# Kernel tuning notes

Hardware: AMD Instinct MI355X
Metric: run time of the kernel (lower is better)

## Reference

```python
import jax, jax.numpy as jnp
import numpy as np

N_NODES = 100000
N_EDGES = 1600000


def setup_inputs() -> dict:
    key = jax.random.key(0)
    ks = jax.random.split(key, 6)
    x = jax.random.normal(ks[0], (N_NODES, 128), dtype=jnp.float32)
    edge_index = jax.random.randint(ks[1], (2, N_EDGES), 0, N_NODES, dtype=jnp.int64)
    # glorot-ish scaled weights
    W0 = jax.random.normal(ks[2], (128, 64), dtype=jnp.float32) * (1.0 / np.sqrt(128))
    W1 = jax.random.normal(ks[3], (64, 64), dtype=jnp.float32) * (1.0 / np.sqrt(64))
    W2 = jax.random.normal(ks[4], (64, 40), dtype=jnp.float32) * (1.0 / np.sqrt(64))
    b0 = jnp.zeros((64,), jnp.float32)
    b1 = jnp.zeros((64,), jnp.float32)
    b2 = jnp.zeros((40,), jnp.float32)
    return {"x": x, "edge_index": edge_index, "W0": W0, "b0": b0,
            "W1": W1, "b1": b1, "W2": W2, "b2": b2}


def _gcn_norm(edge_index, n, dtype):
    # PyG gcn_norm: add self-loops, deg over targets, norm = d^-1/2[src]*d^-1/2[dst]
    loop = jnp.arange(n, dtype=edge_index.dtype)
    src = jnp.concatenate([edge_index[0], loop])
    dst = jnp.concatenate([edge_index[1], loop])
    deg = jax.ops.segment_sum(jnp.ones_like(dst, dtype=dtype), dst, num_segments=n)
    dinv = jnp.where(deg > 0, jax.lax.rsqrt(deg), 0.0)
    return src, dst, dinv[src] * dinv[dst]


def reference(x, edge_index, W0, b0, W1, b1, W2, b2):
    n = x.shape[0]
    src, dst, norm = _gcn_norm(edge_index, n, x.dtype)

    def conv(h, W, b):
        h = h @ W                                   # [N, out]
        msg = h[src] * norm[:, None]                # gather + per-edge scale
        return jax.ops.segment_sum(msg, dst, num_segments=n) + b

    # dropout skipped (eval mode); relu between layers per forward()
    h = jax.nn.relu(conv(x, W0, b0))
    h = jax.nn.relu(conv(h, W1, b1))
    return conv(h, W2, b2)
```

## Files before the change

### kernel.cpp

```cpp
#include <hip/hip_runtime.h>
#include <hip/hip_fp16.h>


#define ALIGN256(x) (((size_t)(x) + 255) & ~(size_t)255)

typedef _Float16 f16;
typedef f16 f16x8 __attribute__((ext_vector_type(8)));
typedef float f32x4 __attribute__((ext_vector_type(4)));


__global__ __launch_bounds__(256) void k_coarse(const int* __restrict__ ei,
                                                int* __restrict__ ccnt,
                                                int* __restrict__ done,
                                                int* __restrict__ cbase,
                                                int* __restrict__ cpos,
                                                int* __restrict__ row_start,
                                                int E, int N, int NBUK, int nblk) {
    __shared__ int h[512];
    __shared__ int lastblk;
    int t = threadIdx.x;
    for (int i = t; i < NBUK; i += 256) h[i] = 0;
    __syncthreads();
    int e0 = blockIdx.x * 8192;
    int e1 = min(e0 + 8192, E);
    for (int e = e0 + t; e < e1; e += 256) atomicAdd(&h[ei[E + e] >> 8], 1);
    __syncthreads();
    for (int i = t; i < NBUK; i += 256) {
        int c = h[i];
        if (c) atomicAdd(&ccnt[i], c);
    }
    __threadfence();
    if (t == 0) lastblk = (atomicAdd(done, 1) == nblk - 1) ? 1 : 0;
    __syncthreads();
    if (!lastblk) return;

    __shared__ int sd[256];
    int i0 = 2 * t, i1 = 2 * t + 1;
    int v0 = (i0 < NBUK) ? ccnt[i0] : 0;
    int v1 = (i1 < NBUK) ? ccnt[i1] : 0;
    int s = v0 + v1;
    sd[t] = s;
    __syncthreads();
    for (int off = 1; off < 256; off <<= 1) {
        int u = (t >= off) ? sd[t - off] : 0;
        __syncthreads();
        sd[t] += u;
        __syncthreads();
    }
    int base = sd[t] - s;
    if (i0 < NBUK) { cbase[i0] = base;      cpos[i0] = base; }
    if (i1 < NBUK) { cbase[i1] = base + v0; cpos[i1] = base + v0; }
    if (t == 0) { cbase[NBUK] = E; row_start[N] = E; }
}


__global__ __launch_bounds__(256) void k_passA(const int* __restrict__ ei,
                                               int* __restrict__ cpos,
                                               unsigned int* __restrict__ stage,
                                               int E, int NBUK) {
    __shared__ int h[512];
    __shared__ int base[512];
    int t = threadIdx.x;
    for (int i = t; i < NBUK; i += 256) h[i] = 0;
    __syncthreads();
    int e0 = blockIdx.x * 8192;
    int e1 = min(e0 + 8192, E);
    for (int e = e0 + t; e < e1; e += 256) atomicAdd(&h[ei[E + e] >> 8], 1);
    __syncthreads();
    for (int b = t; b < NBUK; b += 256) {
        int c = h[b];
        base[b] = c ? atomicAdd(&cpos[b], c) : 0;
        h[b] = 0;
    }
    __syncthreads();
    for (int e = e0 + t; e < e1; e += 256) {
        unsigned int s = (unsigned int)ei[e];
        int d = ei[E + e];
        int b = d >> 8;
        int off = base[b] + atomicAdd(&h[b], 1);
        stage[off] = ((unsigned int)(d & 255) << 24) | s;
    }
}


__global__ __launch_bounds__(256) void k_B1(const unsigned int* __restrict__ stage,
                                            const int* __restrict__ cbase,
                                            int* __restrict__ row_start,
                                            float* __restrict__ dinv, int N) {
    __shared__ int cnt[256];
    __shared__ int sd[256];
    int b = blockIdx.x;
    int n0 = b << 8;
    int t = threadIdx.x;
    cnt[t] = 0;
    __syncthreads();
    int s0 = cbase[b], s1 = cbase[b + 1];
    for (int j = s0 + t; j < s1; j += 256) atomicAdd(&cnt[stage[j] >> 24], 1);
    __syncthreads();
    int c = cnt[t];
    sd[t] = c;
    __syncthreads();
    for (int off = 1; off < 256; off <<= 1) {
        int u = (t >= off) ? sd[t - off] : 0;
        __syncthreads();
        sd[t] += u;
        __syncthreads();
    }
    int excl = sd[t] - c;
    int node = n0 + t;
    if (node < N) {
        row_start[node] = s0 + excl;
        dinv[node] = 1.0f / sqrtf((float)(c + 1));
    }
}


__global__ __launch_bounds__(256) void k_B2(const unsigned int* __restrict__ stage,
                                            const int* __restrict__ cbase,
                                            const int* __restrict__ row_start,
                                            const float* __restrict__ dinv,
                                            int2* __restrict__ ep, int N) {
    __shared__ int lpos[256];
    __shared__ float ld[256];
    int b = blockIdx.x;
    int n0 = b << 8;
    int t = threadIdx.x;
    int node = n0 + t;
    if (node < N) {
        lpos[t] = row_start[node];
        ld[t] = dinv[node];
    }
    __syncthreads();
    int s0 = cbase[b], s1 = cbase[b + 1];
    for (int j = s0 + t; j < s1; j += 256) {
        unsigned int v = stage[j];
        int li = v >> 24;
        int src = v & 0xFFFFFF;
        int slot = atomicAdd(&lpos[li], 1);
        ep[slot] = make_int2(src, __float_as_int(dinv[src] * ld[li]));
    }
}


template <int K, int OUT, int NF, typename XT>
__global__ __launch_bounds__(256) void k_mgemm(const XT* __restrict__ X,
                                               const float* __restrict__ W,
                                               __half* __restrict__ Y, int N) {
    constexpr int NC = NF * 16;
    constexpr int NT = K / 32;
    __shared__ f16 Wl[NT * NF * 4 * 128];

    int tid = threadIdx.x;
    for (int idx = tid; idx < K * NC; idx += 256) {
        int k = idx / NC;
        int n = idx - k * NC;
        float v = (n < OUT) ? W[k * OUT + n] : 0.0f;
        int t = k >> 5, h = (k >> 3) & 3, j = k & 7, f = n >> 4, nn = n & 15;
        Wl[((t * NF + f) * 4 + h) * 128 + nn * 8 + j] = (f16)v;
    }
    __syncthreads();

    int lane = tid & 63;
    int wid = tid >> 6;
    int h = lane >> 4;
    int nn = lane & 15;
    int row = blockIdx.x * 64 + (wid << 4) + nn;
    bool valid = row < N;

    f16x8 xf[NT];
    if (valid) {
        if constexpr (sizeof(XT) == 4) {
            float4 u[NT][2];
            const float* xb = (const float*)X + (size_t)row * K + (h << 3);
#pragma unroll
            for (int t = 0; t < NT; ++t) {
                u[t][0] = *(const float4*)(xb + (t << 5));
                u[t][1] = *(const float4*)(xb + (t << 5) + 4);
            }
#pragma unroll
            for (int t = 0; t < NT; ++t) {
                xf[t][0] = (f16)u[t][0].x; xf[t][1] = (f16)u[t][0].y;
                xf[t][2] = (f16)u[t][0].z; xf[t][3] = (f16)u[t][0].w;
                xf[t][4] = (f16)u[t][1].x; xf[t][5] = (f16)u[t][1].y;
                xf[t][6] = (f16)u[t][1].z; xf[t][7] = (f16)u[t][1].w;
            }
        } else {
            const __half* xb = (const __half*)X + (size_t)row * K + (h << 3);
#pragma unroll
            for (int t = 0; t < NT; ++t)
                xf[t] = *(const f16x8*)(xb + (t << 5));
        }
    } else {
#pragma unroll
        for (int t = 0; t < NT; ++t)
#pragma unroll
            for (int j = 0; j < 8; ++j) xf[t][j] = (f16)0.f;
    }

    f32x4 acc[NF];
#pragma unroll
    for (int f = 0; f < NF; ++f) acc[f] = (f32x4){0.f, 0.f, 0.f, 0.f};

#pragma unroll
    for (int t = 0; t < NT; ++t) {
#pragma unroll
        for (int f = 0; f < NF; ++f) {
            f16x8 wf = *(const f16x8*)&Wl[((t * NF + f) * 4 + h) * 128 + nn * 8];
            acc[f] = __builtin_amdgcn_mfma_f32_16x16x32_f16(wf, xf[t], acc[f], 0, 0, 0);
        }
    }

    if (valid) {
#pragma unroll
        for (int f = 0; f < NF; ++f) {
            int c = (f << 4) + (h << 2);
            if (c < OUT) {
                __half2 p0 = __floats2half2_rn(acc[f][0], acc[f][1]);
                __half2 p1 = __floats2half2_rn(acc[f][2], acc[f][3]);
                uint2 pk = make_uint2(*(unsigned int*)&p0, *(unsigned int*)&p1);
                *(uint2*)&Y[(size_t)row * OUT + c] = pk;
            }
        }
    }
}


__device__ __forceinline__ void fma8(float4& a0, float4& a1, uint4 hv, float w) {
    __half2* hp = (__half2*)&hv;
    float2 f0 = __half22float2(hp[0]);
    float2 f1 = __half22float2(hp[1]);
    float2 f2 = __half22float2(hp[2]);
    float2 f3 = __half22float2(hp[3]);
    a0.x += f0.x * w; a0.y += f0.y * w; a0.z += f1.x * w; a0.w += f1.y * w;
    a1.x += f2.x * w; a1.y += f2.y * w; a1.z += f3.x * w; a1.w += f3.y * w;
}

template <int NV, int F, int RELU, typename OutT>
__global__ __launch_bounds__(256) void k_agg(const __half* __restrict__ H,
                                             const int* __restrict__ row_start,
                                             const int2* __restrict__ ep,
                                             const float* __restrict__ dinv,
                                             const float* __restrict__ bias,
                                             OutT* __restrict__ out, int N) {
    int tid = threadIdx.x;
    int lane = tid & 63;
    int sub = lane >> 3;
    int lq = lane & 7;
    int node = blockIdx.x * 32 + (tid >> 6) * 8 + sub;
    if (node >= N) return;
    const bool act = (NV == 8) || (lq < NV);

    int jb = row_start[node];
    int je = row_start[node + 1];
    float dv = dinv[node];

    float4 a0 = make_float4(0.f, 0.f, 0.f, 0.f);
    float4 a1 = make_float4(0.f, 0.f, 0.f, 0.f);
    if (act) {
        uint4 hv = *(const uint4*)&H[(size_t)node * F + 8 * lq];
        fma8(a0, a1, hv, dv * dv);
    }

    int j = jb;
    for (; j + 8 <= je; j += 8) {
        int2 e0 = ep[j],     e1 = ep[j + 1], e2 = ep[j + 2], e3 = ep[j + 3];
        int2 e4 = ep[j + 4], e5 = ep[j + 5], e6 = ep[j + 6], e7 = ep[j + 7];
        if (act) {
            uint4 h0 = *(const uint4*)&H[(size_t)e0.x * F + 8 * lq];
            uint4 h1 = *(const uint4*)&H[(size_t)e1.x * F + 8 * lq];
            uint4 h2 = *(const uint4*)&H[(size_t)e2.x * F + 8 * lq];
            uint4 h3 = *(const uint4*)&H[(size_t)e3.x * F + 8 * lq];
            uint4 h4 = *(const uint4*)&H[(size_t)e4.x * F + 8 * lq];
            uint4 h5 = *(const uint4*)&H[(size_t)e5.x * F + 8 * lq];
            uint4 h6 = *(const uint4*)&H[(size_t)e6.x * F + 8 * lq];
            uint4 h7 = *(const uint4*)&H[(size_t)e7.x * F + 8 * lq];
            fma8(a0, a1, h0, __int_as_float(e0.y));
            fma8(a0, a1, h1, __int_as_float(e1.y));
            fma8(a0, a1, h2, __int_as_float(e2.y));
            fma8(a0, a1, h3, __int_as_float(e3.y));
            fma8(a0, a1, h4, __int_as_float(e4.y));
            fma8(a0, a1, h5, __int_as_float(e5.y));
            fma8(a0, a1, h6, __int_as_float(e6.y));
            fma8(a0, a1, h7, __int_as_float(e7.y));
        }
    }
    for (; j + 2 <= je; j += 2) {
        int2 e0 = ep[j], e1 = ep[j + 1];
        if (act) {
            uint4 h0 = *(const uint4*)&H[(size_t)e0.x * F + 8 * lq];
            uint4 h1 = *(const uint4*)&H[(size_t)e1.x * F + 8 * lq];
            fma8(a0, a1, h0, __int_as_float(e0.y));
            fma8(a0, a1, h1, __int_as_float(e1.y));
        }
    }
    if (j < je) {
        int2 e = ep[j];
        if (act) {
            uint4 h = *(const uint4*)&H[(size_t)e.x * F + 8 * lq];
            fma8(a0, a1, h, __int_as_float(e.y));
        }
    }

    if (act) {
        float4 b0 = *(const float4*)&bias[8 * lq];
        float4 b1 = *(const float4*)&bias[8 * lq + 4];
        a0.x += b0.x; a0.y += b0.y; a0.z += b0.z; a0.w += b0.w;
        a1.x += b1.x; a1.y += b1.y; a1.z += b1.z; a1.w += b1.w;
        if (RELU) {
            a0.x = fmaxf(a0.x, 0.f); a0.y = fmaxf(a0.y, 0.f);
            a0.z = fmaxf(a0.z, 0.f); a0.w = fmaxf(a0.w, 0.f);
            a1.x = fmaxf(a1.x, 0.f); a1.y = fmaxf(a1.y, 0.f);
            a1.z = fmaxf(a1.z, 0.f); a1.w = fmaxf(a1.w, 0.f);
        }
        if constexpr (sizeof(OutT) == 2) {
            __half2 p0 = __floats2half2_rn(a0.x, a0.y);
            __half2 p1 = __floats2half2_rn(a0.z, a0.w);
            __half2 p2 = __floats2half2_rn(a1.x, a1.y);
            __half2 p3 = __floats2half2_rn(a1.z, a1.w);
            uint4 pk = make_uint4(*(unsigned int*)&p0, *(unsigned int*)&p1,
                                  *(unsigned int*)&p2, *(unsigned int*)&p3);
            *(uint4*)&out[(size_t)node * F + 8 * lq] = pk;
        } else {
            *(float4*)&out[(size_t)node * F + 8 * lq] = a0;
            *(float4*)&out[(size_t)node * F + 8 * lq + 4] = a1;
        }
    }
}


extern "C" void kernel_launch(void* const* d_in, const int* in_sizes, int n_in,
                              void* d_out, int out_size, void* d_ws, size_t ws_size,
                              hipStream_t stream) {
    const float* x  = (const float*)d_in[0];
    const int*   ei = (const int*)d_in[1];
    const float* W0 = (const float*)d_in[2];
    const float* b0 = (const float*)d_in[3];
    const float* W1 = (const float*)d_in[4];
    const float* b1 = (const float*)d_in[5];
    const float* W2 = (const float*)d_in[6];
    const float* b2 = (const float*)d_in[7];
    float* out = (float*)d_out;

    const int N = in_sizes[0] / 128;
    const int E = in_sizes[1] / 2;
    const int NBUK = (N + 255) >> 8;

    char* w = (char*)d_ws;
    size_t off = 0;
    int*    ccnt      = (int*)(w + off);    off = ALIGN256(off + (size_t)(NBUK + 1) * 4);
    int*    done      = ccnt + NBUK;
    int*    cbase     = (int*)(w + off);    off = ALIGN256(off + (size_t)(NBUK + 1) * 4);
    int*    cpos      = (int*)(w + off);    off = ALIGN256(off + (size_t)NBUK * 4);
    int*    row_start = (int*)(w + off);    off = ALIGN256(off + (size_t)(N + 1) * 4);
    float*  dinv      = (float*)(w + off);  off = ALIGN256(off + (size_t)N * 4);
    int2*   ep        = (int2*)(w + off);   off = ALIGN256(off + (size_t)E * 8);
    __half* bufH      = (__half*)(w + off); off = ALIGN256(off + (size_t)N * 64 * 2);
    __half* bufG      = (__half*)(w + off); off = ALIGN256(off + (size_t)N * 64 * 2);
    unsigned int* stage = (unsigned int*)bufG;

    const int gGemm = (N + 63) / 64;
    const int gAgg  = (N + 31) / 32;
    const int gPA   = (E + 8191) / 8192;

    hipMemsetAsync(ccnt, 0, (size_t)(NBUK + 1) * 4, stream);
    k_mgemm<128, 64, 4><<<gGemm, 256, 0, stream>>>(x, W0, bufH, N);
    k_coarse<<<gPA, 256, 0, stream>>>(ei, ccnt, done, cbase, cpos, row_start, E, N, NBUK, gPA);
    k_passA<<<gPA, 256, 0, stream>>>(ei, cpos, stage, E, NBUK);
    k_B1<<<NBUK, 256, 0, stream>>>(stage, cbase, row_start, dinv, N);
    k_B2<<<NBUK, 256, 0, stream>>>(stage, cbase, row_start, dinv, ep, N);

    k_agg<8, 64, 1, __half><<<gAgg, 256, 0, stream>>>(bufH, row_start, ep, dinv, b0, bufG, N);
    k_mgemm<64, 64, 4><<<gGemm, 256, 0, stream>>>(bufG, W1, bufH, N);
    k_agg<8, 64, 1, __half><<<gAgg, 256, 0, stream>>>(bufH, row_start, ep, dinv, b1, bufG, N);
    k_mgemm<64, 40, 3><<<gGemm, 256, 0, stream>>>(bufG, W2, bufH, N);
    k_agg<5, 40, 0, float><<<gAgg, 256, 0, stream>>>(bufH, row_start, ep, dinv, b2, out, N);
}
```

Baseline: 312.7 us.

## Fuse aggregation with the following layer's GEMM in one kernel

Adds a kernel that aggregates neighbour features for 64 nodes, applies bias and ReLU, keeps the fp16 result in shared memory, and runs the next layer's MFMA matmul on it before writing out. This replaces two agg+GEMM kernel pairs and removes a round trip of the N×64 intermediate through global memory plus two launches. In exchange it uses more shared memory per block and adds a barrier between the gather phase and the matmul phase, which may lower occupancy for the latency-bound gather.

```diff
diff --git a/kernel.cpp b/kernel.cpp
--- a/kernel.cpp
+++ b/kernel.cpp
@@ -142,6 +142,56 @@
 }
 
 
+__device__ __forceinline__ void fma8(float4& a0, float4& a1, uint4 hv, float w) {
+    __half2* hp = (__half2*)&hv;
+    float2 f0 = __half22float2(hp[0]);
+    float2 f1 = __half22float2(hp[1]);
+    float2 f2 = __half22float2(hp[2]);
+    float2 f3 = __half22float2(hp[3]);
+    a0.x += f0.x * w; a0.y += f0.y * w; a0.z += f1.x * w; a0.w += f1.y * w;
+    a1.x += f2.x * w; a1.y += f2.y * w; a1.z += f3.x * w; a1.w += f3.y * w;
+}
+
+__device__ __forceinline__ void agg_edges(const __half* __restrict__ H,
+                                          const int2* __restrict__ ep,
+                                          int jb, int je, int lq,
+                                          float4& a0, float4& a1) {
+    int j = jb;
+    for (; j + 8 <= je; j += 8) {
+        int2 e0 = ep[j],     e1 = ep[j + 1], e2 = ep[j + 2], e3 = ep[j + 3];
+        int2 e4 = ep[j + 4], e5 = ep[j + 5], e6 = ep[j + 6], e7 = ep[j + 7];
+        uint4 h0 = *(const uint4*)&H[(size_t)e0.x * 64 + 8 * lq];
+        uint4 h1 = *(const uint4*)&H[(size_t)e1.x * 64 + 8 * lq];
+        uint4 h2 = *(const uint4*)&H[(size_t)e2.x * 64 + 8 * lq];
+        uint4 h3 = *(const uint4*)&H[(size_t)e3.x * 64 + 8 * lq];
+        uint4 h4 = *(const uint4*)&H[(size_t)e4.x * 64 + 8 * lq];
+        uint4 h5 = *(const uint4*)&H[(size_t)e5.x * 64 + 8 * lq];
+        uint4 h6 = *(const uint4*)&H[(size_t)e6.x * 64 + 8 * lq];
+        uint4 h7 = *(const uint4*)&H[(size_t)e7.x * 64 + 8 * lq];
+        fma8(a0, a1, h0, __int_as_float(e0.y));
+        fma8(a0, a1, h1, __int_as_float(e1.y));
+        fma8(a0, a1, h2, __int_as_float(e2.y));
+        fma8(a0, a1, h3, __int_as_float(e3.y));
+        fma8(a0, a1, h4, __int_as_float(e4.y));
+        fma8(a0, a1, h5, __int_as_float(e5.y));
+        fma8(a0, a1, h6, __int_as_float(e6.y));
+        fma8(a0, a1, h7, __int_as_float(e7.y));
+    }
+    for (; j + 2 <= je; j += 2) {
+        int2 e0 = ep[j], e1 = ep[j + 1];
+        uint4 h0 = *(const uint4*)&H[(size_t)e0.x * 64 + 8 * lq];
+        uint4 h1 = *(const uint4*)&H[(size_t)e1.x * 64 + 8 * lq];
+        fma8(a0, a1, h0, __int_as_float(e0.y));
+        fma8(a0, a1, h1, __int_as_float(e1.y));
+    }
+    if (j < je) {
+        int2 e = ep[j];
+        uint4 h = *(const uint4*)&H[(size_t)e.x * 64 + 8 * lq];
+        fma8(a0, a1, h, __int_as_float(e.y));
+    }
+}
+
+
 template <int K, int OUT, int NF, typename XT>
 __global__ __launch_bounds__(256) void k_mgemm(const XT* __restrict__ X,
                                                const float* __restrict__ W,
@@ -225,15 +275,99 @@
 }
 
 
-__device__ __forceinline__ void fma8(float4& a0, float4& a1, uint4 hv, float w) {
-    __half2* hp = (__half2*)&hv;
-    float2 f0 = __half22float2(hp[0]);
-    float2 f1 = __half22float2(hp[1]);
-    float2 f2 = __half22float2(hp[2]);
-    float2 f3 = __half22float2(hp[3]);
-    a0.x += f0.x * w; a0.y += f0.y * w; a0.z += f1.x * w; a0.w += f1.y * w;
-    a1.x += f2.x * w; a1.y += f2.y * w; a1.z += f3.x * w; a1.w += f3.y * w;
-}
+template <int OUT, int NF>
+__global__ __launch_bounds__(256) void k_agg_gemm(const __half* __restrict__ H,
+                                                  const int* __restrict__ row_start,
+                                                  const int2* __restrict__ ep,
+                                                  const float* __restrict__ dinv,
+                                                  const float* __restrict__ bias,
+                                                  const float* __restrict__ W,
+                                                  __half* __restrict__ Y, int N) {
+    constexpr int NC = NF * 16;
+    constexpr int NT = 2;
+    __shared__ f16 Wl[NT * NF * 4 * 128];
+    __shared__ f16 Yl[64 * 72];
+
+    int tid = threadIdx.x;
+    for (int idx = tid; idx < 64 * NC; idx += 256) {
+        int k = idx / NC;
+        int n = idx - k * NC;
+        float v = (n < OUT) ? W[k * OUT + n] : 0.0f;
+        int t = k >> 5, hh = (k >> 3) & 3, j = k & 7, f = n >> 4, nn = n & 15;
+        Wl[((t * NF + f) * 4 + hh) * 128 + nn * 8 + j] = (f16)v;
+    }
+
+    int lane = tid & 63;
+    int sub = lane >> 3;
+    int lq = lane & 7;
+    int wid = tid >> 6;
+
+#pragma unroll
+    for (int pass = 0; pass < 2; ++pass) {
+        int lrow = pass * 32 + wid * 8 + sub;
+        int node = blockIdx.x * 64 + lrow;
+        uint4 pk = make_uint4(0, 0, 0, 0);
+        if (node < N) {
+            int jb = row_start[node];
+            int je = row_start[node + 1];
+            float dv = dinv[node];
+            float4 a0 = make_float4(0.f, 0.f, 0.f, 0.f);
+            float4 a1 = make_float4(0.f, 0.f, 0.f, 0.f);
+            uint4 hv = *(const uint4*)&H[(size_t)node * 64 + 8 * lq];
+            fma8(a0, a1, hv, dv * dv);
+            agg_edges(H, ep, jb, je, lq, a0, a1);
+            float4 b0 = *(const float4*)&bias[8 * lq];
+            float4 b1 = *(const float4*)&bias[8 * lq + 4];
+            a0.x += b0.x; a0.y += b0.y; a0.z += b0.z; a0.w += b0.w;
+            a1.x += b1.x; a1.y += b1.y; a1.z += b1.z; a1.w += b1.w;
+            a0.x = fmaxf(a0.x, 0.f); a0.y = fmaxf(a0.y, 0.f);
+            a0.z = fmaxf(a0.z, 0.f); a0.w = fmaxf(a0.w, 0.f);
+            a1.x = fmaxf(a1.x, 0.f); a1.y = fmaxf(a1.y, 0.f);
+            a1.z = fmaxf(a1.z, 0.f); a1.w = fmaxf(a1.w, 0.f);
+            __half2 p0 = __floats2half2_rn(a0.x, a0.y);
+            __half2 p1 = __floats2half2_rn(a0.z, a0.w);
+            __half2 p2 = __floats2half2_rn(a1.x, a1.y);
+            __half2 p3 = __floats2half2_rn(a1.z, a1.w);
+            pk = make_uint4(*(unsigned int*)&p0, *(unsigned int*)&p1,
+                            *(unsigned int*)&p2, *(unsigned int*)&p3);
+        }
+        *(uint4*)&Yl[lrow * 72 + 8 * lq] = pk;
+    }
+    __syncthreads();
+
+    int h = lane >> 4;
+    int nn = lane & 15;
+    int lrow = (wid << 4) + nn;
+    int row = blockIdx.x * 64 + lrow;
+
+    f32x4 acc[NF];
+#pragma unroll
+    for (int f = 0; f < NF; ++f) acc[f] = (f32x4){0.f, 0.f, 0.f, 0.f};
+
+#pragma unroll
+    for (int t = 0; t < NT; ++t) {
+        f16x8 xf = *(const f16x8*)&Yl[lrow * 72 + (t << 5) + (h << 3)];
+#pragma unroll
+        for (int f = 0; f < NF; ++f) {
+            f16x8 wf = *(const f16x8*)&Wl[((t * NF + f) * 4 + h) * 128 + nn * 8];
+            acc[f] = __builtin_amdgcn_mfma_f32_16x16x32_f16(wf, xf, acc[f], 0, 0, 0);
+        }
+    }
+
+    if (row < N) {
+#pragma unroll
+        for (int f = 0; f < NF; ++f) {
+            int c = (f << 4) + (h << 2);
+            if (c < OUT) {
+                __half2 p0 = __floats2half2_rn(acc[f][0], acc[f][1]);
+                __half2 p1 = __floats2half2_rn(acc[f][2], acc[f][3]);
+                uint2 pk = make_uint2(*(unsigned int*)&p0, *(unsigned int*)&p1);
+                *(uint2*)&Y[(size_t)row * OUT + c] = pk;
+            }
+        }
+    }
+}
+
 
 template <int NV, int F, int RELU, typename OutT>
 __global__ __launch_bounds__(256) void k_agg(const __half* __restrict__ H,
@@ -358,9 +492,10 @@
     __half* bufG      = (__half*)(w + off); off = ALIGN256(off + (size_t)N * 64 * 2);
     unsigned int* stage = (unsigned int*)bufG;
 
-    const int gGemm = (N + 63) / 64;
-    const int gAgg  = (N + 31) / 32;
-    const int gPA   = (E + 8191) / 8192;
+    const int gGemm  = (N + 63) / 64;
+    const int gAgg   = (N + 31) / 32;
+    const int gFused = (N + 63) / 64;
+    const int gPA    = (E + 8191) / 8192;
 
     hipMemsetAsync(ccnt, 0, (size_t)(NBUK + 1) * 4, stream);
     k_mgemm<128, 64, 4><<<gGemm, 256, 0, stream>>>(x, W0, bufH, N);
@@ -369,9 +504,7 @@
     k_B1<<<NBUK, 256, 0, stream>>>(stage, cbase, row_start, dinv, N);
     k_B2<<<NBUK, 256, 0, stream>>>(stage, cbase, row_start, dinv, ep, N);
 
-    k_agg<8, 64, 1, __half><<<gAgg, 256, 0, stream>>>(bufH, row_start, ep, dinv, b0, bufG, N);
-    k_mgemm<64, 64, 4><<<gGemm, 256, 0, stream>>>(bufG, W1, bufH, N);
-    k_agg<8, 64, 1, __half><<<gAgg, 256, 0, stream>>>(bufH, row_start, ep, dinv, b1, bufG, N);
-    k_mgemm<64, 40, 3><<<gGemm, 256, 0, stream>>>(bufG, W2, bufH, N);
+    k_agg_gemm<64, 4><<<gFused, 256, 0, stream>>>(bufH, row_start, ep, dinv, b0, W1, bufG, N);
+    k_agg_gemm<40, 3><<<gFused, 256, 0, stream>>>(bufG, row_start, ep, dinv, b1, W2, bufH, N);
     k_agg<5, 40, 0, float><<<gAgg, 256, 0, stream>>>(bufH, row_start, ep, dinv, b2, out, N);
 }
```

After: 309.1 us. No clear change (-1.2%).
